# Kernel tuning notes

Measured on AMD Instinct MI355X. Metric: run time of the kernel, lower is better.

The kernel has to match this reference:

```python
import jax, jax.numpy as jnp
import numpy as np

N_NODES = 50000
N_EDGES = 800000
F_IN = 128
HID = 128
N_GRAPHS = 256


def setup_inputs() -> dict:
    key = jax.random.key(0)
    ks = jax.random.split(key, 12)
    gx = jax.random.normal(ks[0], (N_NODES, F_IN), dtype=jnp.float32)
    edge_index = jax.random.randint(ks[1], (2, N_EDGES), 0, N_NODES, dtype=jnp.int64)
    batch = jnp.sort(jax.random.randint(ks[2], (N_NODES,), 0, N_GRAPHS, dtype=jnp.int64))
    edge_attr = jax.random.uniform(ks[3], (N_EDGES,), dtype=jnp.float32)
    s1 = 1.0 / np.sqrt(F_IN)
    s2 = 1.0 / np.sqrt(HID)
    W1 = jax.random.uniform(ks[4], (F_IN, HID), jnp.float32, -s1, s1)
    b1 = jnp.zeros((HID,), jnp.float32)
    W2 = jax.random.uniform(ks[5], (HID, HID), jnp.float32, -s2, s2)
    b2 = jnp.zeros((HID,), jnp.float32)
    W3 = jax.random.uniform(ks[6], (HID, HID), jnp.float32, -s2, s2)
    b3 = jnp.zeros((HID,), jnp.float32)
    return {"gx": gx, "edge_index": edge_index, "batch": batch, "edge_attr": edge_attr,
            "W1": W1, "b1": b1, "W2": W2, "b2": b2, "W3": W3, "b3": b3}


def _gcn_conv(x, W, b, row, col, edge_weight, n_nodes):
    # PyG GCNConv with add_self_loops=False:
    #   deg[i] = sum of edge_weight over edges with dst == i
    #   norm_e = deg^{-1/2}[row] * w_e * deg^{-1/2}[col]
    #   out[i] = sum_{e: col_e == i} norm_e * (x @ W)[row_e] + b
    deg = jax.ops.segment_sum(edge_weight, col, num_segments=n_nodes)
    dinv = jnp.where(deg > 0, jax.lax.rsqrt(deg), 0.0)
    norm = dinv[row] * edge_weight * dinv[col]  # [E]
    h = x @ W  # [N, H]
    msg = h[row] * norm[:, None]  # [E, H] gather + scale
    out = jax.ops.segment_sum(msg, col, num_segments=n_nodes)  # scatter-add
    return out + b


def reference(gx, edge_index, batch, edge_attr, W1, b1, W2, b2, W3, b3):
    row, col = edge_index[0], edge_index[1]
    n = gx.shape[0]
    # dropout layers are in eval mode (identity) for a deterministic reference
    h = jax.nn.relu(_gcn_conv(gx, W1, b1, row, col, edge_attr, n))
    h = jax.nn.relu(_gcn_conv(h, W2, b2, row, col, edge_attr, n))
    h = _gcn_conv(h, W3, b3, row, col, edge_attr, n)
    readout = jax.ops.segment_sum(h, batch, num_segments=N_GRAPHS)  # global_add_pool
    return h, readout
```

## Files before the change

### kernel.cpp

```cpp
#include <hip/hip_runtime.h>

#define FEAT 128

typedef __attribute__((ext_vector_type(8))) short short8;
typedef __attribute__((ext_vector_type(4))) float f32x4;

__device__ __forceinline__ unsigned int bf16rtn(float f) {
    unsigned int u = __float_as_uint(f);
    return (u + 0x7fffu + ((u >> 16) & 1u)) >> 16;
}
__device__ __forceinline__ float bf16tof(unsigned int h) { return __uint_as_float(h << 16); }
__device__ __forceinline__ float bf16lo(unsigned int v) { return __uint_as_float(v << 16); }
__device__ __forceinline__ float bf16hi(unsigned int v) { return __uint_as_float(v & 0xffff0000u); }

__global__ __launch_bounds__(256) void hist_kernel(const int* __restrict__ col,
                                                   int* __restrict__ ghist,
                                                   int E, int nblk, int nbuck) {
    __shared__ int h[256];
    const int t = threadIdx.x, b = blockIdx.x;
    h[t] = 0;
    __syncthreads();
    const int base = b * 4096;
#pragma unroll
    for (int i = 0; i < 16; ++i) {
        int e = base + i * 256 + t;
        if (e < E) atomicAdd(&h[col[e] >> 8], 1);
    }
    __syncthreads();
    if (t < nbuck) ghist[t * nblk + b] = h[t];
}

__global__ __launch_bounds__(256) void scan_block_kernel(const int* __restrict__ cnt,
                                                         int* __restrict__ out,
                                                         int* __restrict__ bsum, int M) {
    __shared__ int s[256];
    int t = threadIdx.x;
    int i = blockIdx.x * 256 + t;
    int own = (i < M) ? cnt[i] : 0;
    s[t] = own;
    for (int off = 1; off < 256; off <<= 1) {
        __syncthreads();
        int v = (t >= off) ? s[t - off] : 0;
        __syncthreads();
        s[t] += v;
    }
    __syncthreads();
    if (i < M) out[i] = s[t] - own;
    if (t == 255) bsum[blockIdx.x] = s[255];
}

__global__ __launch_bounds__(256) void scan_bsum_kernel(int* __restrict__ bsum, int nb) {
    __shared__ int s[256];
    int t = threadIdx.x;
    int own = (t < nb) ? bsum[t] : 0;
    s[t] = own;
    for (int off = 1; off < 256; off <<= 1) {
        __syncthreads();
        int v = (t >= off) ? s[t - off] : 0;
        __syncthreads();
        s[t] += v;
    }
    __syncthreads();
    if (t < nb) bsum[t] = s[t] - own;
}

__global__ __launch_bounds__(256) void scatter1_kernel(const int* __restrict__ row,
                                                       const int* __restrict__ col,
                                                       const float* __restrict__ ew,
                                                       const int* __restrict__ gsc,
                                                       const int* __restrict__ bsum,
                                                       uint2* __restrict__ bedge,
                                                       int E, int nblk, int nbuck) {
    __shared__ int cur[256];
    const int t = threadIdx.x, b = blockIdx.x;
    if (t < nbuck) {
        int idx = t * nblk + b;
        cur[t] = gsc[idx] + bsum[idx >> 8];
    }
    __syncthreads();
    const int base = b * 4096;
#pragma unroll
    for (int i = 0; i < 16; ++i) {
        int e = base + i * 256 + t;
        if (e < E) {
            int c = col[e];
            int slot = atomicAdd(&cur[c >> 8], 1);
            bedge[slot] = make_uint2(((unsigned)c << 16) | (unsigned)row[e],
                                     __float_as_uint(ew[e]));
        }
    }
}

__global__ __launch_bounds__(256) void bucket_kernel(const uint2* __restrict__ bedge,
                                                     const int* __restrict__ gsc,
                                                     const int* __restrict__ bsum,
                                                     int* __restrict__ rowptr,
                                                     float* __restrict__ dinv,
                                                     uint2* __restrict__ sedge,
                                                     int N, int E, int nblk, int nbuck) {
    __shared__ int lcnt[256];
    __shared__ float lw[256];
    __shared__ int lscan[256];
    __shared__ int lcur[256];
    __shared__ float ldv[256];

    const int d = blockIdx.x, t = threadIdx.x;
    const int i0 = d * nblk;
    const int base = gsc[i0] + bsum[i0 >> 8];
    int end;
    if (d == nbuck - 1) end = E;
    else {
        const int i1 = (d + 1) * nblk;
        end = gsc[i1] + bsum[i1 >> 8];
    }

    lcnt[t] = 0;
    lw[t] = 0.f;
    __syncthreads();
    for (int i = base + t; i < end; i += 256) {
        uint2 p = bedge[i];
        int c = (p.x >> 16) & 255;
        atomicAdd(&lcnt[c], 1);
        atomicAdd(&lw[c], __uint_as_float(p.y));
    }
    __syncthreads();
    int own = lcnt[t];
    lscan[t] = own;
    for (int off = 1; off < 256; off <<= 1) {
        __syncthreads();
        int v = (t >= off) ? lscan[t - off] : 0;
        __syncthreads();
        lscan[t] += v;
    }
    __syncthreads();
    int excl = lscan[t] - own;
    lcur[t] = base + excl;
    float wsum = lw[t];
    float dv = (wsum > 0.f) ? rsqrtf(wsum) : 0.f;
    ldv[t] = dv;
    int node = d * 256 + t;
    if (node < N) {
        rowptr[node] = base + excl;
        dinv[node] = dv;
    }
    if (d == nbuck - 1 && t == 0) rowptr[N] = E;
    __syncthreads();
    for (int i = base + t; i < end; i += 256) {
        uint2 p = bedge[i];
        int c = (p.x >> 16) & 255;
        int slot = atomicAdd(&lcur[c], 1);
        sedge[slot] = make_uint2(p.x & 0xFFFFu,
                                 __float_as_uint(__uint_as_float(p.y) * ldv[c]));
    }
}

__global__ void convw_kernel(const float* __restrict__ W0, const float* __restrict__ W1,
                             const float* __restrict__ W2,
                             unsigned short* __restrict__ Whi, unsigned short* __restrict__ Wlo) {
    int i = blockIdx.x * blockDim.x + threadIdx.x;
    int which = blockIdx.y;
    const float* W = (which == 0) ? W0 : (which == 1) ? W1 : W2;
    int c = i >> 7, k = i & 127;
    float w = W[(size_t)k * FEAT + c];
    unsigned int h = bf16rtn(w);
    size_t off = (size_t)which * 16384 + (size_t)c * FEAT + k;
    Whi[off] = (unsigned short)h;
    Wlo[off] = (unsigned short)bf16rtn(w - bf16tof(h));
}

__global__ __launch_bounds__(256) void gemm_mfma_kernel(
    const float* __restrict__ X,
    const unsigned short* __restrict__ Wthi, const unsigned short* __restrict__ Wtlo,
    const float* __restrict__ dinv,
    unsigned int* __restrict__ hb,
    int N)
{
    __shared__ unsigned short wh[64 * 128];
    __shared__ unsigned short wl[64 * 128];

    const int tid = threadIdx.x;
    const int r0 = blockIdx.x * 64;
    const int cb = blockIdx.y;

#pragma unroll
    for (int it = 0; it < 4; ++it) {
        int idx = it * 256 + tid;
        int c = idx >> 4;
        int k8 = (idx & 15) * 8;
        int sw = k8 ^ ((c & 7) << 3);
        size_t src = (size_t)(cb * 64 + c) * FEAT + k8;
        *(short8*)&wh[c * 128 + sw] = *(const short8*)(Wthi + src);
        *(short8*)&wl[c * 128 + sw] = *(const short8*)(Wtlo + src);
    }
    __syncthreads();

    const int lane = tid & 63;
    const int wv = tid >> 6;
    const int m = lane & 15;
    const int quad = lane >> 4;
    const int arow = wv * 16 + m;
    const int grow = r0 + arow;
    const float* xrow = X + (size_t)grow * FEAT;

    f32x4 acc[4];
#pragma unroll
    for (int ct = 0; ct < 4; ++ct) acc[ct] = (f32x4){0.f, 0.f, 0.f, 0.f};

#pragma unroll
    for (int kt = 0; kt < 4; ++kt) {
        const int k0 = kt * 32 + quad * 8;
        float4 va = make_float4(0.f, 0.f, 0.f, 0.f);
        float4 vb = make_float4(0.f, 0.f, 0.f, 0.f);
        if (grow < N) {
            va = *(const float4*)(xrow + k0);
            vb = *(const float4*)(xrow + k0 + 4);
        }
        unsigned int h0 = bf16rtn(va.x), h1 = bf16rtn(va.y);
        unsigned int h2 = bf16rtn(va.z), h3 = bf16rtn(va.w);
        unsigned int h4 = bf16rtn(vb.x), h5 = bf16rtn(vb.y);
        unsigned int h6 = bf16rtn(vb.z), h7 = bf16rtn(vb.w);
        short8 ah, al;
        ah[0] = (short)h0; ah[1] = (short)h1; ah[2] = (short)h2; ah[3] = (short)h3;
        ah[4] = (short)h4; ah[5] = (short)h5; ah[6] = (short)h6; ah[7] = (short)h7;
        al[0] = (short)bf16rtn(va.x - bf16tof(h0));
        al[1] = (short)bf16rtn(va.y - bf16tof(h1));
        al[2] = (short)bf16rtn(va.z - bf16tof(h2));
        al[3] = (short)bf16rtn(va.w - bf16tof(h3));
        al[4] = (short)bf16rtn(vb.x - bf16tof(h4));
        al[5] = (short)bf16rtn(vb.y - bf16tof(h5));
        al[6] = (short)bf16rtn(vb.z - bf16tof(h6));
        al[7] = (short)bf16rtn(vb.w - bf16tof(h7));
#pragma unroll
        for (int ct = 0; ct < 4; ++ct) {
            int bc = ct * 16 + m;
            int bw = k0 ^ ((bc & 7) << 3);
            short8 bh = *(const short8*)&wh[bc * 128 + bw];
            short8 bl = *(const short8*)&wl[bc * 128 + bw];
            acc[ct] = __builtin_amdgcn_mfma_f32_16x16x32_bf16(ah, bh, acc[ct], 0, 0, 0);
            acc[ct] = __builtin_amdgcn_mfma_f32_16x16x32_bf16(ah, bl, acc[ct], 0, 0, 0);
            acc[ct] = __builtin_amdgcn_mfma_f32_16x16x32_bf16(al, bh, acc[ct], 0, 0, 0);
        }
    }

    const int rbase = wv * 16 + quad * 4;
    const int grb = r0 + rbase;
    float dv0, dv1, dv2, dv3;
    if (grb + 3 < N) {
        float4 d4 = *(const float4*)(dinv + grb);
        dv0 = d4.x; dv1 = d4.y; dv2 = d4.z; dv3 = d4.w;
    } else {
        dv0 = (grb + 0 < N) ? dinv[grb + 0] : 0.f;
        dv1 = (grb + 1 < N) ? dinv[grb + 1] : 0.f;
        dv2 = (grb + 2 < N) ? dinv[grb + 2] : 0.f;
        dv3 = (grb + 3 < N) ? dinv[grb + 3] : 0.f;
    }

    __syncthreads();
    unsigned short* cl = wh;
#pragma unroll
    for (int ct = 0; ct < 4; ++ct) {
        cl[(rbase + 0) * 72 + ct * 16 + m] = (unsigned short)bf16rtn(acc[ct][0] * dv0);
        cl[(rbase + 1) * 72 + ct * 16 + m] = (unsigned short)bf16rtn(acc[ct][1] * dv1);
        cl[(rbase + 2) * 72 + ct * 16 + m] = (unsigned short)bf16rtn(acc[ct][2] * dv2);
        cl[(rbase + 3) * 72 + ct * 16 + m] = (unsigned short)bf16rtn(acc[ct][3] * dv3);
    }
    __syncthreads();
#pragma unroll
    for (int it = 0; it < 2; ++it) {
        int idx = it * 256 + tid;
        int r = idx >> 3;
        int c4 = (idx & 7) * 4;
        int gr = r0 + r;
        if (gr < N) {
            uint4 pv = *(const uint4*)&cl[r * 72 + c4 * 2];
            *(uint4*)(hb + (size_t)gr * 64 + cb * 32 + c4) = pv;
        }
    }
}

template <int RELU>
__global__ __launch_bounds__(256) void agg_kernel(
    const int* __restrict__ rowptr, const uint2* __restrict__ sedge,
    const uint4* __restrict__ hb4,
    const float* __restrict__ bias,
    float* __restrict__ outX, int N)
{
    const int node = blockIdx.x * 4 + (threadIdx.x >> 6);
    if (node >= N) return;
    const int lane = threadIdx.x & 63;
    const int g = lane >> 4;
    const int j = lane & 15;
    const int s = rowptr[node];
    const int e = rowptr[node + 1];

    float a0 = 0.f, a1 = 0.f, a2 = 0.f, a3 = 0.f;
    float a4 = 0.f, a5 = 0.f, a6 = 0.f, a7 = 0.f;

    for (int gb = s; gb < e; gb += 16) {
        uint2 m0, m1, m2, m3;
        if (gb + 16 <= e) {
            m0 = sedge[gb + g];       m1 = sedge[gb + 4 + g];
            m2 = sedge[gb + 8 + g];   m3 = sedge[gb + 12 + g];
        } else {
            const uint2 z = make_uint2(0u, 0u);
            int i0 = gb + g, i1 = gb + 4 + g, i2 = gb + 8 + g, i3 = gb + 12 + g;
            m0 = (i0 < e) ? sedge[i0] : z;
            m1 = (i1 < e) ? sedge[i1] : z;
            m2 = (i2 < e) ? sedge[i2] : z;
            m3 = (i3 < e) ? sedge[i3] : z;
        }
        uint4 v0 = hb4[(size_t)m0.x * 16 + j];
        uint4 v1 = hb4[(size_t)m1.x * 16 + j];
        uint4 v2 = hb4[(size_t)m2.x * 16 + j];
        uint4 v3 = hb4[(size_t)m3.x * 16 + j];
        float w0 = __uint_as_float(m0.y), w1 = __uint_as_float(m1.y);
        float w2 = __uint_as_float(m2.y), w3 = __uint_as_float(m3.y);
        a0 = fmaf(w0, bf16lo(v0.x), a0); a1 = fmaf(w0, bf16hi(v0.x), a1);
        a2 = fmaf(w0, bf16lo(v0.y), a2); a3 = fmaf(w0, bf16hi(v0.y), a3);
        a4 = fmaf(w0, bf16lo(v0.z), a4); a5 = fmaf(w0, bf16hi(v0.z), a5);
        a6 = fmaf(w0, bf16lo(v0.w), a6); a7 = fmaf(w0, bf16hi(v0.w), a7);
        a0 = fmaf(w1, bf16lo(v1.x), a0); a1 = fmaf(w1, bf16hi(v1.x), a1);
        a2 = fmaf(w1, bf16lo(v1.y), a2); a3 = fmaf(w1, bf16hi(v1.y), a3);
        a4 = fmaf(w1, bf16lo(v1.z), a4); a5 = fmaf(w1, bf16hi(v1.z), a5);
        a6 = fmaf(w1, bf16lo(v1.w), a6); a7 = fmaf(w1, bf16hi(v1.w), a7);
        a0 = fmaf(w2, bf16lo(v2.x), a0); a1 = fmaf(w2, bf16hi(v2.x), a1);
        a2 = fmaf(w2, bf16lo(v2.y), a2); a3 = fmaf(w2, bf16hi(v2.y), a3);
        a4 = fmaf(w2, bf16lo(v2.z), a4); a5 = fmaf(w2, bf16hi(v2.z), a5);
        a6 = fmaf(w2, bf16lo(v2.w), a6); a7 = fmaf(w2, bf16hi(v2.w), a7);
        a0 = fmaf(w3, bf16lo(v3.x), a0); a1 = fmaf(w3, bf16hi(v3.x), a1);
        a2 = fmaf(w3, bf16lo(v3.y), a2); a3 = fmaf(w3, bf16hi(v3.y), a3);
        a4 = fmaf(w3, bf16lo(v3.z), a4); a5 = fmaf(w3, bf16hi(v3.z), a5);
        a6 = fmaf(w3, bf16lo(v3.w), a6); a7 = fmaf(w3, bf16hi(v3.w), a7);
    }

    a0 += __shfl_xor(a0, 16); a0 += __shfl_xor(a0, 32);
    a1 += __shfl_xor(a1, 16); a1 += __shfl_xor(a1, 32);
    a2 += __shfl_xor(a2, 16); a2 += __shfl_xor(a2, 32);
    a3 += __shfl_xor(a3, 16); a3 += __shfl_xor(a3, 32);
    a4 += __shfl_xor(a4, 16); a4 += __shfl_xor(a4, 32);
    a5 += __shfl_xor(a5, 16); a5 += __shfl_xor(a5, 32);
    a6 += __shfl_xor(a6, 16); a6 += __shfl_xor(a6, 32);
    a7 += __shfl_xor(a7, 16); a7 += __shfl_xor(a7, 32);

    if (g == 0) {
        float4 bv0 = ((const float4*)bias)[j * 2];
        float4 bv1 = ((const float4*)bias)[j * 2 + 1];
        a0 += bv0.x; a1 += bv0.y; a2 += bv0.z; a3 += bv0.w;
        a4 += bv1.x; a5 += bv1.y; a6 += bv1.z; a7 += bv1.w;
        if (RELU) {
            a0 = fmaxf(a0, 0.f); a1 = fmaxf(a1, 0.f);
            a2 = fmaxf(a2, 0.f); a3 = fmaxf(a3, 0.f);
            a4 = fmaxf(a4, 0.f); a5 = fmaxf(a5, 0.f);
            a6 = fmaxf(a6, 0.f); a7 = fmaxf(a7, 0.f);
        }
        *(float4*)(outX + (size_t)node * FEAT + j * 8)     = make_float4(a0, a1, a2, a3);
        *(float4*)(outX + (size_t)node * FEAT + j * 8 + 4) = make_float4(a4, a5, a6, a7);
    }
}

__global__ __launch_bounds__(256) void readout_kernel(const float* __restrict__ h,
                                                      const int* __restrict__ batch,
                                                      float* __restrict__ ro, int N) {
    __shared__ float part[128];
    const int g = blockIdx.x;
    const int j = threadIdx.x & 127;
    const int half = threadIdx.x >> 7;
    int lo = 0, hi = N;
    while (lo < hi) { int mid = (lo + hi) >> 1; if (batch[mid] < g) lo = mid + 1; else hi = mid; }
    int lo2 = lo, hi2 = N;
    while (lo2 < hi2) { int mid = (lo2 + hi2) >> 1; if (batch[mid] < g + 1) lo2 = mid + 1; else hi2 = mid; }

    float s0 = 0.f, s1 = 0.f;
    int n = lo + half;
    for (; n + 2 < lo2; n += 4) {
        s0 += h[(size_t)n * FEAT + j];
        s1 += h[(size_t)(n + 2) * FEAT + j];
    }
    if (n < lo2) s0 += h[(size_t)n * FEAT + j];
    float s = s0 + s1;
    if (half == 1) part[j] = s;
    __syncthreads();
    if (half == 0) ro[(size_t)g * FEAT + j] = s + part[j];
}

static inline size_t align256(size_t x) { return (x + 255) & ~(size_t)255; }

extern "C" void kernel_launch(void* const* d_in, const int* in_sizes, int n_in,
                              void* d_out, int out_size, void* d_ws, size_t ws_size,
                              hipStream_t stream) {
    const float* gx    = (const float*)d_in[0];
    const int*   ei    = (const int*)d_in[1];
    const int*   batch = (const int*)d_in[2];
    const float* ew    = (const float*)d_in[3];
    const float* W1 = (const float*)d_in[4];
    const float* b1 = (const float*)d_in[5];
    const float* W2 = (const float*)d_in[6];
    const float* b2 = (const float*)d_in[7];
    const float* W3 = (const float*)d_in[8];
    const float* b3 = (const float*)d_in[9];

    const int N = in_sizes[0] / FEAT;
    const int E = in_sizes[3];
    const int G = (out_size - N * FEAT) / FEAT;

    const int* row = ei;
    const int* col = ei + E;

    const int nbuck = (N + 255) >> 8;
    const int nblk  = (E + 4095) >> 12;
    const int M     = nbuck * nblk;

    char* ws = (char*)d_ws;
    int*   rowptr = (int*)ws;         ws += align256((size_t)(N + 1) * 4);
    float* dinv   = (float*)ws;       ws += align256((size_t)N * 4);
    int*   ghist  = (int*)ws;         ws += align256((size_t)M * 4);
    int*   gsc    = (int*)ws;         ws += align256((size_t)M * 4);
    int*   bsum   = (int*)ws;         ws += align256(256 * 4);
    uint2* bedge  = (uint2*)ws;       ws += align256((size_t)E * 8);
    uint2* sedge  = (uint2*)ws;       ws += align256((size_t)E * 8);
    unsigned int* hb = (unsigned int*)ws;  ws += align256((size_t)N * 64 * 4);
    float* bufX   = (float*)ws;       ws += align256((size_t)N * FEAT * 4);
    unsigned short* Wh = (unsigned short*)ws; ws += align256((size_t)3 * 16384 * 2);
    unsigned short* Wl = (unsigned short*)ws; ws += align256((size_t)3 * 16384 * 2);

    float* h_out = (float*)d_out;
    float* ro    = h_out + (size_t)N * FEAT;

    hist_kernel<<<nblk, 256, 0, stream>>>(col, ghist, E, nblk, nbuck);
    const int snb = (M + 255) / 256;
    scan_block_kernel<<<snb, 256, 0, stream>>>(ghist, gsc, bsum, M);
    scan_bsum_kernel<<<1, 256, 0, stream>>>(bsum, snb);
    scatter1_kernel<<<nblk, 256, 0, stream>>>(row, col, ew, gsc, bsum, bedge, E, nblk, nbuck);
    bucket_kernel<<<nbuck, 256, 0, stream>>>(bedge, gsc, bsum, rowptr, dinv, sedge, N, E, nblk, nbuck);

    convw_kernel<<<dim3(64, 3), 256, 0, stream>>>(W1, W2, W3, Wh, Wl);

    dim3 ggrid((N + 63) / 64, 2);
    const int ablocks = (N + 3) / 4;
    const uint4* hb4 = (const uint4*)hb;

    gemm_mfma_kernel<<<ggrid, 256, 0, stream>>>(gx, Wh, Wl, dinv, hb, N);
    agg_kernel<1><<<ablocks, 256, 0, stream>>>(rowptr, sedge, hb4, b1, bufX, N);
    gemm_mfma_kernel<<<ggrid, 256, 0, stream>>>(bufX, Wh + 16384, Wl + 16384, dinv, hb, N);
    agg_kernel<1><<<ablocks, 256, 0, stream>>>(rowptr, sedge, hb4, b2, bufX, N);
    gemm_mfma_kernel<<<ggrid, 256, 0, stream>>>(bufX, Wh + 32768, Wl + 32768, dinv, hb, N);
    agg_kernel<0><<<ablocks, 256, 0, stream>>>(rowptr, sedge, hb4, b3, h_out, N);
    readout_kernel<<<G, 256, 0, stream>>>(h_out, batch, ro, N);
}
```

Before: 289.1 us.

## Map one 16-lane group per node in aggregation, unroll edges by eight

The aggregation kernel now gives each node 16 lanes instead of a full 64-lane wavefront, so one wavefront handles four nodes. Each group walks all of its node's edges serially, eight per iteration, and the cross-group shuffle reduction is gone. This is meant to avoid idle lanes on low-degree nodes (average degree about 16) and to drop the reduction. In exchange there is less parallelism per node and more per-lane work, and the edge records are fetched as broadcast loads, one per lane group.

```diff
diff --git a/kernel.cpp b/kernel.cpp
--- a/kernel.cpp
+++ b/kernel.cpp
@@ -285,36 +285,45 @@
     const float* __restrict__ bias,
     float* __restrict__ outX, int N)
 {
-    const int node = blockIdx.x * 4 + (threadIdx.x >> 6);
+    const int node = blockIdx.x * 16 + (threadIdx.x >> 4);
     if (node >= N) return;
-    const int lane = threadIdx.x & 63;
-    const int g = lane >> 4;
-    const int j = lane & 15;
+    const int j = threadIdx.x & 15;
     const int s = rowptr[node];
     const int e = rowptr[node + 1];
 
     float a0 = 0.f, a1 = 0.f, a2 = 0.f, a3 = 0.f;
     float a4 = 0.f, a5 = 0.f, a6 = 0.f, a7 = 0.f;
 
-    for (int gb = s; gb < e; gb += 16) {
-        uint2 m0, m1, m2, m3;
-        if (gb + 16 <= e) {
-            m0 = sedge[gb + g];       m1 = sedge[gb + 4 + g];
-            m2 = sedge[gb + 8 + g];   m3 = sedge[gb + 12 + g];
+    for (int gb = s; gb < e; gb += 8) {
+        uint2 m0, m1, m2, m3, m4, m5, m6, m7;
+        if (gb + 8 <= e) {
+            m0 = sedge[gb + 0]; m1 = sedge[gb + 1];
+            m2 = sedge[gb + 2]; m3 = sedge[gb + 3];
+            m4 = sedge[gb + 4]; m5 = sedge[gb + 5];
+            m6 = sedge[gb + 6]; m7 = sedge[gb + 7];
         } else {
             const uint2 z = make_uint2(0u, 0u);
-            int i0 = gb + g, i1 = gb + 4 + g, i2 = gb + 8 + g, i3 = gb + 12 + g;
-            m0 = (i0 < e) ? sedge[i0] : z;
-            m1 = (i1 < e) ? sedge[i1] : z;
-            m2 = (i2 < e) ? sedge[i2] : z;
-            m3 = (i3 < e) ? sedge[i3] : z;
+            m0 = (gb + 0 < e) ? sedge[gb + 0] : z;
+            m1 = (gb + 1 < e) ? sedge[gb + 1] : z;
+            m2 = (gb + 2 < e) ? sedge[gb + 2] : z;
+            m3 = (gb + 3 < e) ? sedge[gb + 3] : z;
+            m4 = (gb + 4 < e) ? sedge[gb + 4] : z;
+            m5 = (gb + 5 < e) ? sedge[gb + 5] : z;
+            m6 = (gb + 6 < e) ? sedge[gb + 6] : z;
+            m7 = (gb + 7 < e) ? sedge[gb + 7] : z;
         }
         uint4 v0 = hb4[(size_t)m0.x * 16 + j];
         uint4 v1 = hb4[(size_t)m1.x * 16 + j];
         uint4 v2 = hb4[(size_t)m2.x * 16 + j];
         uint4 v3 = hb4[(size_t)m3.x * 16 + j];
+        uint4 v4 = hb4[(size_t)m4.x * 16 + j];
+        uint4 v5 = hb4[(size_t)m5.x * 16 + j];
+        uint4 v6 = hb4[(size_t)m6.x * 16 + j];
+        uint4 v7 = hb4[(size_t)m7.x * 16 + j];
         float w0 = __uint_as_float(m0.y), w1 = __uint_as_float(m1.y);
         float w2 = __uint_as_float(m2.y), w3 = __uint_as_float(m3.y);
+        float w4 = __uint_as_float(m4.y), w5 = __uint_as_float(m5.y);
+        float w6 = __uint_as_float(m6.y), w7 = __uint_as_float(m7.y);
         a0 = fmaf(w0, bf16lo(v0.x), a0); a1 = fmaf(w0, bf16hi(v0.x), a1);
         a2 = fmaf(w0, bf16lo(v0.y), a2); a3 = fmaf(w0, bf16hi(v0.y), a3);
         a4 = fmaf(w0, bf16lo(v0.z), a4); a5 = fmaf(w0, bf16hi(v0.z), a5);
@@ -331,31 +340,36 @@
         a2 = fmaf(w3, bf16lo(v3.y), a2); a3 = fmaf(w3, bf16hi(v3.y), a3);
         a4 = fmaf(w3, bf16lo(v3.z), a4); a5 = fmaf(w3, bf16hi(v3.z), a5);
         a6 = fmaf(w3, bf16lo(v3.w), a6); a7 = fmaf(w3, bf16hi(v3.w), a7);
-    }
-
-    a0 += __shfl_xor(a0, 16); a0 += __shfl_xor(a0, 32);
-    a1 += __shfl_xor(a1, 16); a1 += __shfl_xor(a1, 32);
-    a2 += __shfl_xor(a2, 16); a2 += __shfl_xor(a2, 32);
-    a3 += __shfl_xor(a3, 16); a3 += __shfl_xor(a3, 32);
-    a4 += __shfl_xor(a4, 16); a4 += __shfl_xor(a4, 32);
-    a5 += __shfl_xor(a5, 16); a5 += __shfl_xor(a5, 32);
-    a6 += __shfl_xor(a6, 16); a6 += __shfl_xor(a6, 32);
-    a7 += __shfl_xor(a7, 16); a7 += __shfl_xor(a7, 32);
-
-    if (g == 0) {
-        float4 bv0 = ((const float4*)bias)[j * 2];
-        float4 bv1 = ((const float4*)bias)[j * 2 + 1];
-        a0 += bv0.x; a1 += bv0.y; a2 += bv0.z; a3 += bv0.w;
-        a4 += bv1.x; a5 += bv1.y; a6 += bv1.z; a7 += bv1.w;
-        if (RELU) {
-            a0 = fmaxf(a0, 0.f); a1 = fmaxf(a1, 0.f);
-            a2 = fmaxf(a2, 0.f); a3 = fmaxf(a3, 0.f);
-            a4 = fmaxf(a4, 0.f); a5 = fmaxf(a5, 0.f);
-            a6 = fmaxf(a6, 0.f); a7 = fmaxf(a7, 0.f);
-        }
-        *(float4*)(outX + (size_t)node * FEAT + j * 8)     = make_float4(a0, a1, a2, a3);
-        *(float4*)(outX + (size_t)node * FEAT + j * 8 + 4) = make_float4(a4, a5, a6, a7);
-    }
+        a0 = fmaf(w4, bf16lo(v4.x), a0); a1 = fmaf(w4, bf16hi(v4.x), a1);
+        a2 = fmaf(w4, bf16lo(v4.y), a2); a3 = fmaf(w4, bf16hi(v4.y), a3);
+        a4 = fmaf(w4, bf16lo(v4.z), a4); a5 = fmaf(w4, bf16hi(v4.z), a5);
+        a6 = fmaf(w4, bf16lo(v4.w), a6); a7 = fmaf(w4, bf16hi(v4.w), a7);
+        a0 = fmaf(w5, bf16lo(v5.x), a0); a1 = fmaf(w5, bf16hi(v5.x), a1);
+        a2 = fmaf(w5, bf16lo(v5.y), a2); a3 = fmaf(w5, bf16hi(v5.y), a3);
+        a4 = fmaf(w5, bf16lo(v5.z), a4); a5 = fmaf(w5, bf16hi(v5.z), a5);
+        a6 = fmaf(w5, bf16lo(v5.w), a6); a7 = fmaf(w5, bf16hi(v5.w), a7);
+        a0 = fmaf(w6, bf16lo(v6.x), a0); a1 = fmaf(w6, bf16hi(v6.x), a1);
+        a2 = fmaf(w6, bf16lo(v6.y), a2); a3 = fmaf(w6, bf16hi(v6.y), a3);
+        a4 = fmaf(w6, bf16lo(v6.z), a4); a5 = fmaf(w6, bf16hi(v6.z), a5);
+        a6 = fmaf(w6, bf16lo(v6.w), a6); a7 = fmaf(w6, bf16hi(v6.w), a7);
+        a0 = fmaf(w7, bf16lo(v7.x), a0); a1 = fmaf(w7, bf16hi(v7.x), a1);
+        a2 = fmaf(w7, bf16lo(v7.y), a2); a3 = fmaf(w7, bf16hi(v7.y), a3);
+        a4 = fmaf(w7, bf16lo(v7.z), a4); a5 = fmaf(w7, bf16hi(v7.z), a5);
+        a6 = fmaf(w7, bf16lo(v7.w), a6); a7 = fmaf(w7, bf16hi(v7.w), a7);
+    }
+
+    float4 bv0 = ((const float4*)bias)[j * 2];
+    float4 bv1 = ((const float4*)bias)[j * 2 + 1];
+    a0 += bv0.x; a1 += bv0.y; a2 += bv0.z; a3 += bv0.w;
+    a4 += bv1.x; a5 += bv1.y; a6 += bv1.z; a7 += bv1.w;
+    if (RELU) {
+        a0 = fmaxf(a0, 0.f); a1 = fmaxf(a1, 0.f);
+        a2 = fmaxf(a2, 0.f); a3 = fmaxf(a3, 0.f);
+        a4 = fmaxf(a4, 0.f); a5 = fmaxf(a5, 0.f);
+        a6 = fmaxf(a6, 0.f); a7 = fmaxf(a7, 0.f);
+    }
+    *(float4*)(outX + (size_t)node * FEAT + j * 8)     = make_float4(a0, a1, a2, a3);
+    *(float4*)(outX + (size_t)node * FEAT + j * 8 + 4) = make_float4(a4, a5, a6, a7);
 }
 
 __global__ __launch_bounds__(256) void readout_kernel(const float* __restrict__ h,
@@ -436,7 +450,7 @@
     convw_kernel<<<dim3(64, 3), 256, 0, stream>>>(W1, W2, W3, Wh, Wl);
 
     dim3 ggrid((N + 63) / 64, 2);
-    const int ablocks = (N + 3) / 4;
+    const int ablocks = (N + 15) / 16;
     const uint4* hb4 = (const uint4*)hb;
 
     gemm_mfma_kernel<<<ggrid, 256, 0, stream>>>(gx, Wh, Wl, dinv, hb, N);
```

Result: no change. 285.7 us (-1.2%).
